# Kernel tuning notes

Hardware: AMD Instinct MI355X
Metric: run time of the kernel (lower is better)

Reference implementation:

```python
import jax, jax.numpy as jnp
import numpy as np

N = 50000
E = 800000
IN_DIM = 128
HID = 64
OUT_DIM = 1
NEG_SLOPE = 0.2
EPS = 1e-16


def _glorot(key, shape):
    fan = shape[-1] + (shape[0] if len(shape) > 1 else shape[-1])
    lim = jnp.sqrt(6.0 / fan)
    return jax.random.uniform(key, shape, jnp.float32, -lim, lim)


def setup_inputs() -> dict:
    key = jax.random.key(0)
    ks = jax.random.split(key, 12)
    x = jax.random.normal(ks[0], (N, IN_DIM), jnp.float32)
    edge_index = jax.random.randint(ks[1], (2, E), 0, N, jnp.int64)
    # GATConv layer 1: in=128, out=64, heads=4, concat=True
    W1 = _glorot(ks[2], (4 * HID, IN_DIM))
    att_src1 = _glorot(ks[3], (4, HID))
    att_dst1 = _glorot(ks[4], (4, HID))
    b1 = jnp.zeros((4 * HID,), jnp.float32)
    # GATConv layer 2: in=256, out=64, heads=1, concat=True
    W2 = _glorot(ks[5], (HID, 4 * HID))
    att_src2 = _glorot(ks[6], (1, HID))
    att_dst2 = _glorot(ks[7], (1, HID))
    b2 = jnp.zeros((HID,), jnp.float32)
    # final Linear(hidden, 1)
    fc_w = _glorot(ks[8], (OUT_DIM, HID))
    fc_b = jnp.zeros((OUT_DIM,), jnp.float32)
    return {"x": x, "edge_index": edge_index, "W1": W1, "att_src1": att_src1,
            "att_dst1": att_dst1, "b1": b1, "W2": W2, "att_src2": att_src2,
            "att_dst2": att_dst2, "b2": b2, "fc_w": fc_w, "fc_b": fc_b}


def _gat_layer(x, src, dst, W, att_src, att_dst, bias, heads, out_ch):
    n = x.shape[0]
    xt = (x @ W.T).reshape(n, heads, out_ch)          # [N, H, C]
    a_src = jnp.sum(xt * att_src[None], axis=-1)      # [N, H]
    a_dst = jnp.sum(xt * att_dst[None], axis=-1)      # [N, H]
    e = a_src[src] + a_dst[dst]                       # [E', H]
    e = jnp.where(e > 0, e, NEG_SLOPE * e)            # LeakyReLU(0.2)
    # segment softmax over incoming edges of each dst node
    m = jax.ops.segment_max(e, dst, num_segments=n)
    e = jnp.exp(e - m[dst])
    s = jax.ops.segment_sum(e, dst, num_segments=n)
    alpha = e / (s[dst] + EPS)                        # [E', H]
    msg = xt[src] * alpha[:, :, None]                 # [E', H, C]
    out = jax.ops.segment_sum(msg, dst, num_segments=n)
    return out.reshape(n, heads * out_ch) + bias


def reference(x, edge_index, W1, att_src1, att_dst1, b1,
              W2, att_src2, att_dst2, b2, fc_w, fc_b):
    n = x.shape[0]
    # PyG GATConv default: add self-loops
    loops = jnp.arange(n, dtype=edge_index.dtype)
    src = jnp.concatenate([edge_index[0], loops])
    dst = jnp.concatenate([edge_index[1], loops])
    h = jax.nn.relu(_gat_layer(x, src, dst, W1, att_src1, att_dst1, b1, 4, HID))
    h = jax.nn.relu(_gat_layer(h, src, dst, W2, att_src2, att_dst2, b2, 1, HID))
    logits = h @ fc_w.T + fc_b                        # [N, 1]
    return jax.nn.sigmoid(logits).squeeze()
```

## Files before the change

### kernel.cpp

```cpp
#include <hip/hip_runtime.h>
#include <hip/hip_bf16.h>

#define NN 50000
#define EE 800000
#define ET (NN + EE)
#define SG ((NN + 255) / 256)
#define GB1 ((NN + 63) / 64)

typedef __attribute__((ext_vector_type(8))) short short8;
typedef __attribute__((ext_vector_type(4))) float f32x4;

__device__ __forceinline__ float bf2f(unsigned short u) {
    union { unsigned int i; float f; } v; v.i = ((unsigned int)u) << 16; return v.f;
}
__device__ __forceinline__ unsigned short f2bf(float f) {
    __hip_bfloat16 h = __float2bfloat16(f);
    return *reinterpret_cast<unsigned short*>(&h);
}
__device__ __forceinline__ float lrelu(float e) { return e > 0.f ? e : 0.2f * e; }


__global__ void k_hist(const int* __restrict__ dst, int* __restrict__ cnt) {
    int i = blockIdx.x * blockDim.x + threadIdx.x;
    if (i < EE) atomicAdd(&cnt[dst[i]], 1);
}

__global__ __launch_bounds__(256) void k_scanprep(
    const int* __restrict__ cnt, unsigned long long* __restrict__ lb,
    int* __restrict__ rowptr, int* __restrict__ writeptr, int* __restrict__ csr)
{
    int b = blockIdx.x, t = threadIdx.x, i = b * 256 + t;
    int lane = t & 63, w = t >> 6;
    int v = (i < NN) ? cnt[i] : 0;
    int s = v;
    #pragma unroll
    for (int off = 1; off < 64; off <<= 1) {
        int u = __shfl_up(s, off);
        if (lane >= off) s += u;
    }
    __shared__ int ws[4];
    __shared__ int prev_sh;
    if (lane == 63) ws[w] = s;
    __syncthreads();
    if (t == 0) {
        int a = 0;
        #pragma unroll
        for (int k = 0; k < 4; k++) { int x = ws[k]; ws[k] = a; a += x; }
        unsigned long long pk =
            ((unsigned long long)(b == 0 ? 2u : 1u) << 32) | (unsigned int)a;
        atomicExch(&lb[b], pk);
        if (b == 0) prev_sh = 0;
    }
    __syncthreads();

    if (w == 0 && b > 0) {
        int prev = 0;
        int j = b - 1;
        while (true) {
            int idx = j - lane;
            bool active = (idx >= 0);
            int st = 0, val = 0;
            while (true) {
                if (active && st == 0) {
                    unsigned long long got = atomicAdd(&lb[idx], 0ULL);
                    st = (int)(got >> 32);
                    val = (int)(got & 0xffffffffULL);
                }
                if (!__any(active && st == 0)) break;
            }
            unsigned long long incmask = __ballot(active && st == 2);
            if (incmask) {
                int L = __ffsll(incmask) - 1;
                int contrib = (active && lane <= L) ? val : 0;
                #pragma unroll
                for (int off = 32; off; off >>= 1) contrib += __shfl_xor(contrib, off);
                prev += contrib;
                break;
            } else {
                int contrib = active ? val : 0;
                #pragma unroll
                for (int off = 32; off; off >>= 1) contrib += __shfl_xor(contrib, off);
                prev += contrib;
                j -= 64;
            }
        }
        if (lane == 0) {
            prev_sh = prev;
            unsigned long long mine = atomicAdd(&lb[b], 0ULL);
            int tot = (int)(mine & 0xffffffffULL);
            atomicExch(&lb[b], (2ULL << 32) | (unsigned int)(prev + tot));
        }
    }
    __syncthreads();
    int prev = prev_sh;

    if (i == 0) rowptr[0] = 0;
    if (i < NN) {
        int incl_e = prev + ws[w] + s;
        int excl_e = incl_e - v;
        rowptr[i + 1] = incl_e + i + 1;
        int excl = excl_e + i;
        csr[excl] = i;
        writeptr[i] = excl + 1;
    }
}

template<int K, int N, int NH, bool A_BF16>
__device__ __forceinline__ void gemm_body(
    int bid, const void* __restrict__ Aptr, const float* __restrict__ W,
    const float* __restrict__ atts, const float* __restrict__ attd,
    unsigned short* __restrict__ C, float* __restrict__ as_, float* __restrict__ ad_,
    int M)
{
    constexpr int KU  = K / 8;
    constexpr int KUH = KU / 2;
    constexpr int KC  = K / 32;
    constexpr int NW  = N / 4;
    constexpr int NI  = NW / 16;
    constexpr int ABYTES = 64 * KU * 16;
    constexpr int BBYTES = N * KUH * 16;
    constexpr int SMEM = ABYTES + BBYTES + (NH == 1 ? 2048 : 0);
    __shared__ char smem[SMEM];
    char* Ash = smem;
    char* Bsh = smem + ABYTES;
    unsigned short* Csh = (unsigned short*)smem;
    float* scsh = (float*)(smem + ABYTES + BBYTES);

    int t = threadIdx.x;
    int lane = t & 63, w = t >> 6;
    int colL = lane & 15, quad = lane >> 4;
    int m0 = bid * 64;

    {
        constexpr int CNT = 64 * KU / 256;
        #pragma unroll
        for (int i = 0; i < CNT; i++) {
            int v = t + 256 * i;
            int m = v / KU, u = v % KU;
            int gr = m0 + m; if (gr >= M) gr = M - 1;
            short8 val;
            if (A_BF16) {
                val = *(const short8*)((const unsigned short*)Aptr + (size_t)gr * K + u * 8);
            } else {
                const float* Af = (const float*)Aptr;
                float4 lo = *(const float4*)(Af + (size_t)gr * K + u * 8);
                float4 hi = *(const float4*)(Af + (size_t)gr * K + u * 8 + 4);
                val[0] = (short)f2bf(lo.x); val[1] = (short)f2bf(lo.y);
                val[2] = (short)f2bf(lo.z); val[3] = (short)f2bf(lo.w);
                val[4] = (short)f2bf(hi.x); val[5] = (short)f2bf(hi.y);
                val[6] = (short)f2bf(hi.z); val[7] = (short)f2bf(hi.w);
            }
            *(short8*)(Ash + ((size_t)m * KU + (u ^ (m & 7))) * 16) = val;
        }
    }

    f32x4 acc[4][NI];
    #pragma unroll
    for (int mi = 0; mi < 4; mi++)
        #pragma unroll
        for (int ni = 0; ni < NI; ni++) acc[mi][ni] = (f32x4){0.f, 0.f, 0.f, 0.f};

    #pragma unroll
    for (int kh = 0; kh < 2; kh++) {
        __syncthreads();
        {
            constexpr int CNT = N * KUH / 256;
            #pragma unroll
            for (int i = 0; i < CNT; i++) {
                int v = t + 256 * i;
                int n = v / KUH, uu = v % KUH;
                int u = kh * KUH + uu;
                float4 lo = *(const float4*)(W + (size_t)n * K + u * 8);
                float4 hi = *(const float4*)(W + (size_t)n * K + u * 8 + 4);
                short8 val;
                val[0] = (short)f2bf(lo.x); val[1] = (short)f2bf(lo.y);
                val[2] = (short)f2bf(lo.z); val[3] = (short)f2bf(lo.w);
                val[4] = (short)f2bf(hi.x); val[5] = (short)f2bf(hi.y);
                val[6] = (short)f2bf(hi.z); val[7] = (short)f2bf(hi.w);
                *(short8*)(Bsh + ((size_t)n * KUH + (uu ^ (n & 7))) * 16) = val;
            }
        }
        __syncthreads();
        #pragma unroll
        for (int kcl = 0; kcl < KC / 2; kcl++) {
            int uA = (kh * (KC / 2) + kcl) * 4 + quad;
            int uB = kcl * 4 + quad;
            short8 bf[NI];
            #pragma unroll
            for (int ni = 0; ni < NI; ni++) {
                int n = w * NW + ni * 16 + colL;
                bf[ni] = *(const short8*)(Bsh + ((size_t)n * KUH + (uB ^ (n & 7))) * 16);
            }
            #pragma unroll
            for (int mi = 0; mi < 4; mi++) {
                int m = mi * 16 + colL;
                short8 af = *(const short8*)(Ash + ((size_t)m * KU + (uA ^ (m & 7))) * 16);
                #pragma unroll
                for (int ni = 0; ni < NI; ni++)
                    acc[mi][ni] = __builtin_amdgcn_mfma_f32_16x16x32_bf16(af, bf[ni], acc[mi][ni], 0, 0, 0);
            }
        }
    }
    __syncthreads();

    float asv[NI], adv[NI];
    #pragma unroll
    for (int ni = 0; ni < NI; ni++) {
        int na = (NH == 4) ? (w * 64 + ni * 16 + colL) : (w * 16 + colL);
        asv[ni] = atts[na];
        adv[ni] = attd[na];
    }
    #pragma unroll
    for (int mi = 0; mi < 4; mi++) {
        float ps[4] = {0.f, 0.f, 0.f, 0.f}, pd[4] = {0.f, 0.f, 0.f, 0.f};
        #pragma unroll
        for (int ni = 0; ni < NI; ni++)
            #pragma unroll
            for (int r = 0; r < 4; r++) {
                ps[r] += acc[mi][ni][r] * asv[ni];
                pd[r] += acc[mi][ni][r] * adv[ni];
            }
        #pragma unroll
        for (int off = 1; off < 16; off <<= 1)
            #pragma unroll
            for (int r = 0; r < 4; r++) {
                ps[r] += __shfl_xor(ps[r], off);
                pd[r] += __shfl_xor(pd[r], off);
            }
        if (colL == 0) {
            #pragma unroll
            for (int r = 0; r < 4; r++) {
                int rloc = mi * 16 + quad * 4 + r;
                if (NH == 4) {
                    int row = m0 + rloc;
                    if (row < M) {
                        as_[(size_t)row * 4 + w] = ps[r];
                        ad_[(size_t)row * 4 + w] = pd[r];
                    }
                } else {
                    scsh[(w * 64 + rloc) * 2 + 0] = ps[r];
                    scsh[(w * 64 + rloc) * 2 + 1] = pd[r];
                }
            }
        }
    }

    #pragma unroll
    for (int mi = 0; mi < 4; mi++)
        #pragma unroll
        for (int ni = 0; ni < NI; ni++)
            #pragma unroll
            for (int r = 0; r < 4; r++)
                Csh[(size_t)(mi * 16 + quad * 4 + r) * (N + 8) + w * NW + ni * 16 + colL] =
                    f2bf(acc[mi][ni][r]);
    __syncthreads();

    {
        constexpr int CNT = 64 * (N / 8) / 256;
        #pragma unroll
        for (int i = 0; i < CNT; i++) {
            int v = t + 256 * i;
            int m = v / (N / 8), u = v % (N / 8);
            int row = m0 + m;
            if (row < M)
                *(short8*)(C + (size_t)row * N + u * 8) =
                    *(const short8*)(Csh + (size_t)m * (N + 8) + u * 8);
        }
    }
    if (NH == 1 && t < 64) {
        int row = m0 + t;
        if (row < M) {
            float s = 0.f, d = 0.f;
            #pragma unroll
            for (int ww = 0; ww < 4; ww++) {
                s += scsh[(ww * 64 + t) * 2 + 0];
                d += scsh[(ww * 64 + t) * 2 + 1];
            }
            as_[row] = s;
            ad_[row] = d;
        }
    }
}

template<int K, int N, int NH, bool A_BF16>
__global__ __launch_bounds__(256) void k_gemm_mfma(
    const void* __restrict__ Aptr, const float* __restrict__ W,
    const float* __restrict__ atts, const float* __restrict__ attd,
    unsigned short* __restrict__ C, float* __restrict__ as_, float* __restrict__ ad_,
    int M)
{
    gemm_body<K, N, NH, A_BF16>(blockIdx.x, Aptr, W, atts, attd, C, as_, ad_, M);
}

__global__ __launch_bounds__(256) void k_gemm1_scatter(
    const void* __restrict__ Aptr, const float* __restrict__ W,
    const float* __restrict__ atts, const float* __restrict__ attd,
    unsigned short* __restrict__ C, float* __restrict__ as_, float* __restrict__ ad_,
    int M,
    const int* __restrict__ src, const int* __restrict__ dst,
    int* __restrict__ writeptr, int* __restrict__ csr)
{
    int bid = blockIdx.x;
    int g = bid / 5, r = bid % 5;
    if (r == 0 && g < GB1) {
        gemm_body<128, 256, 4, false>(g, Aptr, W, atts, attd, C, as_, ad_, M);
    } else {
        int ng = (r == 0) ? g : g + 1;
        if (ng > GB1) ng = GB1;
        int sb = bid - ng;
        int i = sb * 256 + threadIdx.x;
        if (i < EE) {
            int pos = atomicAdd(&writeptr[dst[i]], 1);
            csr[pos] = src[i];
        }
    }
}

__global__ __launch_bounds__(256) void k_l1_agg(
    const unsigned short* __restrict__ xt1, const float* __restrict__ as1,
    const float* __restrict__ ad1, const int* __restrict__ rowptr,
    const int* __restrict__ csr, const float* __restrict__ b1,
    unsigned short* __restrict__ h1)
{
    int t = threadIdx.x;
    int lane = t & 63, w = t >> 6;
    int n = blockIdx.x * 4 + w;
    int beg = rowptr[n], deg = rowptr[n + 1] - beg;
    int half = lane >> 5, c = lane & 31, h = c >> 3;
    float adh = ad1[n * 4 + h];

    float acc[8] = {0.f, 0.f, 0.f, 0.f, 0.f, 0.f, 0.f, 0.f};
    float esum = 0.f;
    int j = 0;
    for (; j + 4 <= deg; j += 4) {
        int p = beg + j + half * 2;
        int s0 = csr[p], s1 = csr[p + 1];
        float e0 = __expf(lrelu(as1[s0 * 4 + h] + adh));
        float e1 = __expf(lrelu(as1[s1 * 4 + h] + adh));
        short8 r0 = *(const short8*)(xt1 + (size_t)s0 * 256 + c * 8);
        short8 r1 = *(const short8*)(xt1 + (size_t)s1 * 256 + c * 8);
        esum += e0 + e1;
        #pragma unroll
        for (int k = 0; k < 8; k++)
            acc[k] += bf2f((unsigned short)r0[k]) * e0 + bf2f((unsigned short)r1[k]) * e1;
    }
    for (; j < deg; j += 2) {
        int jj = j + half;
        if (jj < deg) {
            int p = beg + jj;
            int s = csr[p];
            float e = __expf(lrelu(as1[s * 4 + h] + adh));
            short8 r = *(const short8*)(xt1 + (size_t)s * 256 + c * 8);
            esum += e;
            #pragma unroll
            for (int k = 0; k < 8; k++) acc[k] += bf2f((unsigned short)r[k]) * e;
        }
    }
    #pragma unroll
    for (int k = 0; k < 8; k++) acc[k] += __shfl_xor(acc[k], 32);
    esum += __shfl_xor(esum, 32);
    if (half == 0) {
        float rs = 1.f / (esum + 1e-16f);
        float4 bl = *(const float4*)(b1 + c * 8);
        float4 bh = *(const float4*)(b1 + c * 8 + 4);
        float bb[8] = {bl.x, bl.y, bl.z, bl.w, bh.x, bh.y, bh.z, bh.w};
        short8 o;
        #pragma unroll
        for (int k = 0; k < 8; k++)
            o[k] = (short)f2bf(fmaxf(acc[k] * rs + bb[k], 0.f));
        *(short8*)(h1 + (size_t)n * 256 + c * 8) = o;
    }
}

__global__ __launch_bounds__(256) void k_l2_agg(
    const unsigned short* __restrict__ xt2, const float* __restrict__ as2,
    const float* __restrict__ ad2, const int* __restrict__ rowptr,
    const int* __restrict__ csr, const float* __restrict__ b2,
    const float* __restrict__ fcw, const float* __restrict__ fcb,
    float* __restrict__ out)
{
    int t = threadIdx.x;
    int lane = t & 63, w = t >> 6;
    int n = blockIdx.x * 4 + w;
    int beg = rowptr[n], deg = rowptr[n + 1] - beg;
    int half = lane >> 5, c = lane & 31;
    float adv = ad2[n];

    float a0 = 0.f, a1 = 0.f, esum = 0.f;
    int j = 0;
    for (; j + 4 <= deg; j += 4) {
        int p = beg + j + half * 2;
        int s0 = csr[p], s1 = csr[p + 1];
        float e0 = __expf(lrelu(as2[s0] + adv));
        float e1 = __expf(lrelu(as2[s1] + adv));
        unsigned int r0 = *(const unsigned int*)(xt2 + (size_t)s0 * 64 + c * 2);
        unsigned int r1 = *(const unsigned int*)(xt2 + (size_t)s1 * 64 + c * 2);
        esum += e0 + e1;
        a0 += bf2f(r0 & 0xffff) * e0 + bf2f(r1 & 0xffff) * e1;
        a1 += bf2f(r0 >> 16) * e0 + bf2f(r1 >> 16) * e1;
    }
    for (; j < deg; j += 2) {
        int jj = j + half;
        if (jj < deg) {
            int p = beg + jj;
            int s = csr[p];
            float e = __expf(lrelu(as2[s] + adv));
            unsigned int r = *(const unsigned int*)(xt2 + (size_t)s * 64 + c * 2);
            esum += e;
            a0 += bf2f(r & 0xffff) * e;
            a1 += bf2f(r >> 16) * e;
        }
    }
    a0 += __shfl_xor(a0, 32);
    a1 += __shfl_xor(a1, 32);
    esum += __shfl_xor(esum, 32);
    if (half == 0) {
        float rs = 1.f / (esum + 1e-16f);
        float o0 = fmaxf(a0 * rs + b2[c * 2], 0.f);
        float o1 = fmaxf(a1 * rs + b2[c * 2 + 1], 0.f);
        float z = o0 * fcw[c * 2] + o1 * fcw[c * 2 + 1];
        #pragma unroll
        for (int off = 16; off; off >>= 1) z += __shfl_xor(z, off);
        if (c == 0) out[n] = 1.f / (1.f + __expf(-(z + fcb[0])));
    }
}


extern "C" void kernel_launch(void* const* d_in, const int* in_sizes, int n_in,
                              void* d_out, int out_size, void* d_ws, size_t ws_size,
                              hipStream_t stream) {
    const float* x    = (const float*)d_in[0];
    const int*   ei   = (const int*)d_in[1];
    const float* W1   = (const float*)d_in[2];
    const float* as1w = (const float*)d_in[3];
    const float* ad1w = (const float*)d_in[4];
    const float* b1   = (const float*)d_in[5];
    const float* W2   = (const float*)d_in[6];
    const float* as2w = (const float*)d_in[7];
    const float* ad2w = (const float*)d_in[8];
    const float* b2   = (const float*)d_in[9];
    const float* fcw  = (const float*)d_in[10];
    const float* fcb  = (const float*)d_in[11];
    float* out = (float*)d_out;

    const int* src = ei;
    const int* dst = ei + EE;

    char* base = (char*)d_ws;
    size_t off = 0;
    auto alloc = [&](size_t bytes) -> void* {
        void* p = base + off;
        off = (off + bytes + 255) & ~(size_t)255;
        return p;
    };
    int*   rowptr   = (int*)alloc((NN + 1) * sizeof(int));
    int*   cnt      = (int*)alloc(NN * sizeof(int) + 2048);
    unsigned long long* lb =
        (unsigned long long*)((char*)cnt + ((NN * sizeof(int) + 255) & ~(size_t)255));
    int*   writeptr = (int*)alloc(NN * sizeof(int));
    int*   csr      = (int*)alloc(ET * sizeof(int));
    unsigned short* xt1 = (unsigned short*)alloc((size_t)NN * 256 * sizeof(unsigned short));
    unsigned short* h1  = (unsigned short*)alloc((size_t)NN * 256 * sizeof(unsigned short));
    float* as1      = (float*)alloc(NN * 4 * sizeof(float));
    float* ad1      = (float*)alloc(NN * 4 * sizeof(float));
    float* as2      = (float*)alloc(NN * sizeof(float));
    float* ad2      = (float*)alloc(NN * sizeof(float));
    unsigned short* xt2 = xt1;

    hipMemsetAsync(cnt, 0, NN * sizeof(int) + 2048, stream);
    k_hist<<<(EE + 255) / 256, 256, 0, stream>>>(dst, cnt);
    k_scanprep<<<SG, 256, 0, stream>>>(cnt, lb, rowptr, writeptr, csr);

    int fused_blocks = GB1 + (EE + 255) / 256;
    k_gemm1_scatter<<<fused_blocks, 256, 0, stream>>>(
        x, W1, as1w, ad1w, xt1, as1, ad1, NN, src, dst, writeptr, csr);

    k_l1_agg<<<NN / 4, 256, 0, stream>>>(xt1, as1, ad1, rowptr, csr, b1, h1);
    k_gemm_mfma<256, 64, 1, true><<<GB1, 256, 0, stream>>>(
        h1, W2, as2w, ad2w, xt2, as2, ad2, NN);
    k_l2_agg<<<NN / 4, 256, 0, stream>>>(xt2, as2, ad2, rowptr, csr, b2, fcw, fcb, out);
}
```

Baseline: 290.1 us.

## Vectorize histogram, shrink GEMM B staging, widen layer-2 aggregation gathers

The histogram kernel now reads destination indices as int2 pairs, so it launches half as many threads, each issuing two atomics. The GEMM stages the weight matrix in four K-quarters instead of two, which cuts the B tile in shared memory, and it drops the padded C staging stride. This lowers LDS use and may allow more resident blocks, at the cost of extra barriers and possible bank conflicts on the unpadded C writes. The layer-2 aggregation has each lane load four bf16 values and processes four edges per iteration across 16-lane groups, which changes gather width and the reduction pattern.

New measurement: 292.5 us. Within noise of the previous version (+0.8%).

```diff
diff --git a/kernel.cpp b/kernel.cpp
--- a/kernel.cpp
+++ b/kernel.cpp
@@ -20,9 +20,13 @@
 __device__ __forceinline__ float lrelu(float e) { return e > 0.f ? e : 0.2f * e; }
 
 
-__global__ void k_hist(const int* __restrict__ dst, int* __restrict__ cnt) {
+__global__ void k_hist(const int2* __restrict__ dst2, int* __restrict__ cnt) {
     int i = blockIdx.x * blockDim.x + threadIdx.x;
-    if (i < EE) atomicAdd(&cnt[dst[i]], 1);
+    if (i < EE / 2) {
+        int2 d = dst2[i];
+        atomicAdd(&cnt[d.x], 1);
+        atomicAdd(&cnt[d.y], 1);
+    }
 }
 
 __global__ __launch_bounds__(256) void k_scanprep(
@@ -113,18 +117,21 @@
     int M)
 {
     constexpr int KU  = K / 8;
-    constexpr int KUH = KU / 2;
+    constexpr int KUQ = KU / 4;
     constexpr int KC  = K / 32;
+    constexpr int KCQ = KC / 4;
     constexpr int NW  = N / 4;
     constexpr int NI  = NW / 16;
     constexpr int ABYTES = 64 * KU * 16;
-    constexpr int BBYTES = N * KUH * 16;
-    constexpr int SMEM = ABYTES + BBYTES + (NH == 1 ? 2048 : 0);
+    constexpr int BBYTES = N * KUQ * 16;
+    constexpr int CSHB = 64 * N * 2;
+    constexpr int STG = ABYTES + BBYTES;
+    constexpr int SMEM = (CSHB > STG ? CSHB : STG) + (NH == 1 ? 2048 : 0);
     __shared__ char smem[SMEM];
     char* Ash = smem;
     char* Bsh = smem + ABYTES;
     unsigned short* Csh = (unsigned short*)smem;
-    float* scsh = (float*)(smem + ABYTES + BBYTES);
+    float* scsh = (float*)(smem + (CSHB > STG ? CSHB : STG));
 
     int t = threadIdx.x;
     int lane = t & 63, w = t >> 6;
@@ -161,15 +168,15 @@
         for (int ni = 0; ni < NI; ni++) acc[mi][ni] = (f32x4){0.f, 0.f, 0.f, 0.f};
 
     #pragma unroll
-    for (int kh = 0; kh < 2; kh++) {
+    for (int kh = 0; kh < 4; kh++) {
         __syncthreads();
         {
-            constexpr int CNT = N * KUH / 256;
+            constexpr int CNT = N * KUQ / 256;
             #pragma unroll
             for (int i = 0; i < CNT; i++) {
                 int v = t + 256 * i;
-                int n = v / KUH, uu = v % KUH;
-                int u = kh * KUH + uu;
+                int n = v / KUQ, uu = v % KUQ;
+                int u = kh * KUQ + uu;
                 float4 lo = *(const float4*)(W + (size_t)n * K + u * 8);
                 float4 hi = *(const float4*)(W + (size_t)n * K + u * 8 + 4);
                 short8 val;
@@ -177,19 +184,19 @@
                 val[2] = (short)f2bf(lo.z); val[3] = (short)f2bf(lo.w);
                 val[4] = (short)f2bf(hi.x); val[5] = (short)f2bf(hi.y);
                 val[6] = (short)f2bf(hi.z); val[7] = (short)f2bf(hi.w);
-                *(short8*)(Bsh + ((size_t)n * KUH + (uu ^ (n & 7))) * 16) = val;
+                *(short8*)(Bsh + ((size_t)n * KUQ + (uu ^ (n & (KUQ - 1)))) * 16) = val;
             }
         }
         __syncthreads();
         #pragma unroll
-        for (int kcl = 0; kcl < KC / 2; kcl++) {
-            int uA = (kh * (KC / 2) + kcl) * 4 + quad;
+        for (int kcl = 0; kcl < KCQ; kcl++) {
+            int uA = (kh * KCQ + kcl) * 4 + quad;
             int uB = kcl * 4 + quad;
             short8 bf[NI];
             #pragma unroll
             for (int ni = 0; ni < NI; ni++) {
                 int n = w * NW + ni * 16 + colL;
-                bf[ni] = *(const short8*)(Bsh + ((size_t)n * KUH + (uB ^ (n & 7))) * 16);
+                bf[ni] = *(const short8*)(Bsh + ((size_t)n * KUQ + (uB ^ (n & (KUQ - 1)))) * 16);
             }
             #pragma unroll
             for (int mi = 0; mi < 4; mi++) {
@@ -251,7 +258,7 @@
         for (int ni = 0; ni < NI; ni++)
             #pragma unroll
             for (int r = 0; r < 4; r++)
-                Csh[(size_t)(mi * 16 + quad * 4 + r) * (N + 8) + w * NW + ni * 16 + colL] =
+                Csh[(size_t)(mi * 16 + quad * 4 + r) * N + w * NW + ni * 16 + colL] =
                     f2bf(acc[mi][ni][r]);
     __syncthreads();
 
@@ -264,7 +271,7 @@
             int row = m0 + m;
             if (row < M)
                 *(short8*)(C + (size_t)row * N + u * 8) =
-                    *(const short8*)(Csh + (size_t)m * (N + 8) + u * 8);
+                    *(const short8*)(Csh + (size_t)m * N + u * 8);
         }
     }
     if (NH == 1 && t < 64) {
@@ -382,45 +389,42 @@
     int t = threadIdx.x;
     int lane = t & 63, w = t >> 6;
     int n = blockIdx.x * 4 + w;
-    int beg = rowptr[n], deg = rowptr[n + 1] - beg;
-    int half = lane >> 5, c = lane & 31;
+    int beg = rowptr[n], end = rowptr[n + 1];
+    int q = lane >> 4, c = lane & 15;
     float adv = ad2[n];
 
-    float a0 = 0.f, a1 = 0.f, esum = 0.f;
-    int j = 0;
-    for (; j + 4 <= deg; j += 4) {
-        int p = beg + j + half * 2;
-        int s0 = csr[p], s1 = csr[p + 1];
-        float e0 = __expf(lrelu(as2[s0] + adv));
-        float e1 = __expf(lrelu(as2[s1] + adv));
-        unsigned int r0 = *(const unsigned int*)(xt2 + (size_t)s0 * 64 + c * 2);
-        unsigned int r1 = *(const unsigned int*)(xt2 + (size_t)s1 * 64 + c * 2);
-        esum += e0 + e1;
-        a0 += bf2f(r0 & 0xffff) * e0 + bf2f(r1 & 0xffff) * e1;
-        a1 += bf2f(r0 >> 16) * e0 + bf2f(r1 >> 16) * e1;
-    }
-    for (; j < deg; j += 2) {
-        int jj = j + half;
-        if (jj < deg) {
-            int p = beg + jj;
-            int s = csr[p];
-            float e = __expf(lrelu(as2[s] + adv));
-            unsigned int r = *(const unsigned int*)(xt2 + (size_t)s * 64 + c * 2);
-            esum += e;
-            a0 += bf2f(r & 0xffff) * e;
-            a1 += bf2f(r >> 16) * e;
-        }
-    }
-    a0 += __shfl_xor(a0, 32);
-    a1 += __shfl_xor(a1, 32);
-    esum += __shfl_xor(esum, 32);
-    if (half == 0) {
+    float a0 = 0.f, a1 = 0.f, a2 = 0.f, a3 = 0.f, esum = 0.f;
+    for (int p0 = beg; p0 < end; p0 += 4) {
+        int p = p0 + q;
+        int pc = min(p, end - 1);
+        int s = csr[pc];
+        float e = __expf(lrelu(as2[s] + adv));
+        if (p >= end) e = 0.f;
+        ushort4 r = *(const ushort4*)(xt2 + (size_t)s * 64 + c * 4);
+        esum += e;
+        a0 += bf2f(r.x) * e;
+        a1 += bf2f(r.y) * e;
+        a2 += bf2f(r.z) * e;
+        a3 += bf2f(r.w) * e;
+    }
+    #pragma unroll
+    for (int off = 16; off < 64; off <<= 1) {
+        a0 += __shfl_xor(a0, off);
+        a1 += __shfl_xor(a1, off);
+        a2 += __shfl_xor(a2, off);
+        a3 += __shfl_xor(a3, off);
+        esum += __shfl_xor(esum, off);
+    }
+    if (q == 0) {
         float rs = 1.f / (esum + 1e-16f);
-        float o0 = fmaxf(a0 * rs + b2[c * 2], 0.f);
-        float o1 = fmaxf(a1 * rs + b2[c * 2 + 1], 0.f);
-        float z = o0 * fcw[c * 2] + o1 * fcw[c * 2 + 1];
-        #pragma unroll
-        for (int off = 16; off; off >>= 1) z += __shfl_xor(z, off);
+        float o0 = fmaxf(a0 * rs + b2[c * 4 + 0], 0.f);
+        float o1 = fmaxf(a1 * rs + b2[c * 4 + 1], 0.f);
+        float o2 = fmaxf(a2 * rs + b2[c * 4 + 2], 0.f);
+        float o3 = fmaxf(a3 * rs + b2[c * 4 + 3], 0.f);
+        float z = o0 * fcw[c * 4 + 0] + o1 * fcw[c * 4 + 1]
+                + o2 * fcw[c * 4 + 2] + o3 * fcw[c * 4 + 3];
+        #pragma unroll
+        for (int off = 8; off; off >>= 1) z += __shfl_xor(z, off);
         if (c == 0) out[n] = 1.f / (1.f + __expf(-(z + fcb[0])));
     }
 }
@@ -468,7 +472,7 @@
     unsigned short* xt2 = xt1;
 
     hipMemsetAsync(cnt, 0, NN * sizeof(int) + 2048, stream);
-    k_hist<<<(EE + 255) / 256, 256, 0, stream>>>(dst, cnt);
+    k_hist<<<(EE / 2 + 255) / 256, 256, 0, stream>>>((const int2*)dst, cnt);
     k_scanprep<<<SG, 256, 0, stream>>>(cnt, lb, rowptr, writeptr, csr);
 
     int fused_blocks = GB1 + (EE + 255) / 256;
```
